# Performance work log

Measured on AMD Instinct MI355X. Metric: run time of the kernel, lower is better.

Reference implementation:

```python
import jax, jax.numpy as jnp
import numpy as np

B, L, D, K = 32, 200, 768, 8  # batch, seq_len, bert dim, max_span_length
S = int(sum(L - 1 - k for k in range(1, K + 1)))  # 1556 total spans for a full sentence


def setup_inputs() -> dict:
    key = jax.random.key(0)
    ks = jax.random.split(key, 20)
    features = jax.random.normal(ks[0], (B, L, D), dtype=jnp.float32)
    lengths = jax.random.randint(ks[1], (B,), K + 4, L + 1)  # valid token counts incl CLS/SEP
    mask = (jnp.arange(L)[None, :] < lengths[:, None]).astype(jnp.int32)
    span_mask = jnp.ones((B, S), dtype=jnp.int32)
    inp = {"features": features, "mask": mask, "span_mask": span_mask}
    for j in range(K - 1):
        k = j + 2
        inp[f"w{k}"] = jax.random.normal(ks[2 + j], (D, D, k), dtype=jnp.float32) * 0.02
        inp[f"b{k}"] = jax.random.normal(ks[10 + j], (D,), dtype=jnp.float32) * 0.02
    return inp


def _feature_slice(features, mask, num_spans, ws, bs):
    # features: [B, L, D]; mask: [B, L] (ones then zeros); ws[j]: Conv1d weight [D, D, j+2]
    Bb, Ll, Dd = features.shape
    Kk = len(ws) + 1  # max_span_length
    x = features.transpose(0, 2, 1)  # [B, D, L] (NCH)
    sources = [features]  # k=0: unigram features
    for w, b in zip(ws, bs):
        y = jax.lax.conv_general_dilated(x, w, (1,), "VALID", dimension_numbers=("NCH", "OIH", "NCH"))
        y = (y + b[None, :, None]).transpose(0, 2, 1)  # [B, L-k+1, D]
        sources.append(jnp.pad(y, ((0, 0), (0, Ll - y.shape[1]), (0, 0))))
    src = jnp.stack(sources, 0)  # [K, B, L, D]
    n = jnp.sum(mask, axis=1)  # valid lengths incl CLS/SEP
    # span-length k+1 contributes max(n - k - 2, 0) spans, sources start at index 1
    counts = jnp.maximum(n[:, None] - jnp.arange(Kk)[None, :] - 2, 0)  # [B, K]
    offsets = jnp.concatenate([jnp.zeros((Bb, 1), counts.dtype), jnp.cumsum(counts, axis=1)], axis=1)  # [B, K+1]
    s = jnp.arange(num_spans)
    kidx = jnp.sum(offsets[:, 1:Kk, None] <= s[None, None, :], axis=1)  # [B, S] bucket per slot
    pos = jnp.clip(s[None, :] - jnp.take_along_axis(offsets, kidx, axis=1) + 1, 0, Ll - 1)  # [B, S]
    valid = s[None, :] < offsets[:, Kk:Kk + 1]  # [B, S]
    out = src[kidx, jnp.arange(Bb)[:, None], pos] * valid[:, :, None].astype(features.dtype)
    return out, valid.astype(jnp.int32)


def reference(features, mask, span_mask, w2, w3, w4, w5, w6, w7, w8, b2, b3, b4, b5, b6, b7, b8):
    ws = (w2, w3, w4, w5, w6, w7, w8)
    bs = (b2, b3, b4, b5, b6, b7, b8)
    return _feature_slice(features, mask, span_mask.shape[1], ws, bs)
```

## Files before the change

### kernel.cpp

```cpp
#include <hip/hip_runtime.h>
#include <hip/hip_bf16.h>

#define BB 32
#define LL 200
#define DD 768
#define SS 1556
#define MAXM 6400

typedef __attribute__((ext_vector_type(8))) short bf16x8;
typedef __attribute__((ext_vector_type(4))) float floatx4;

__device__ __forceinline__ float bf2f(ushort u){
    union { unsigned int i; float f; } v; v.i = ((unsigned int)u) << 16; return v.f;
}
__device__ __forceinline__ ushort f2bf(float f){
    union { float f; unsigned int i; } v; v.f = f;
    unsigned int x = v.i;
    return (ushort)((x + 0x7FFFu + ((x >> 16) & 1u)) >> 16);
}

__device__ const int GCNT2[8] = {2,2,2,2,2,2,4,5};
__device__ const int GLIST2[8][5] = {
    {18, 9, 0, 0, 0},
    {19,10, 0, 0, 0},
    {20,11, 0, 0, 0},
    {15,12, 0, 0, 0},
    {16,13, 0, 0, 0},
    {17,14, 0, 0, 0},
    { 6, 7, 3, 0, 0},
    { 8, 4, 5, 1, 2},
};

__global__ void detect_kernel(const unsigned int* __restrict__ feat_raw, int* __restrict__ flag){
    __shared__ int cnt_s;
    if (threadIdx.x == 0) cnt_s = 0;
    __syncthreads();
    int c = 0;
    for (int i = threadIdx.x; i < 4096; i += 256){
        unsigned int w = feat_raw[i];
        unsigned int e = (w >> 7) & 0xFFu;
        if (e >= 100u && e <= 150u) c++;
    }
    atomicAdd(&cnt_s, c);
    __syncthreads();
    if (threadIdx.x == 0) *flag = (cnt_s > 2457) ? 1 : 0;
}

__global__ void offs_kernel(const int* __restrict__ mask, int* __restrict__ offs){
    int b = blockIdx.x;
    int lane = threadIdx.x;
    int s = 0;
    for (int i = lane; i < LL; i += 64) s += mask[b*LL + i];
    #pragma unroll
    for (int d = 32; d > 0; d >>= 1) s += __shfl_down(s, d, 64);
    if (lane == 0){
        int n = s, cum = 0;
        offs[b*9 + 0] = 0;
        for (int j = 0; j < 8; ++j){
            int c = n - j - 2; if (c < 0) c = 0;
            cum += c;
            offs[b*9 + j + 1] = cum;
        }
    }
}

__global__ void maps_kernel(const int* __restrict__ offs, int* __restrict__ pfx,
                            int* __restrict__ amap, int* __restrict__ omap){
    const int kkidx = blockIdx.x;
    const int kk = kkidx + 2;
    __shared__ int P[33];
    __shared__ int base_s[32];
    const int tid = threadIdx.x;
    if (tid == 0){
        int acc = 0; P[0] = 0;
        for (int b = 0; b < 32; ++b){
            acc += offs[b*9 + kk] - offs[b*9 + kk - 1];
            P[b+1] = acc;
        }
    }
    if (tid < 32) base_s[tid] = offs[tid*9 + kk - 1];
    __syncthreads();
    if (tid == 0) pfx[kkidx*33 + 32] = P[32];
    const int Mtot = P[32];
    for (int r = tid; r < MAXM; r += 256){
        int b = 0;
        #pragma unroll
        for (int i = 1; i <= 32; ++i) b += (P[i] <= r) ? 1 : 0;
        int bb = b < 32 ? b : 31;
        int larow = (r < Mtot) ? (r - P[bb]) : 0;
        amap[kkidx*MAXM + r] = bb*LL + larow + 1;
        omap[kkidx*MAXM + r] = bb*SS + base_s[bb] + larow;
    }
}

__global__ void repack2_kernel(const void* __restrict__ w2, const void* __restrict__ w3,
                               const void* __restrict__ w4, const void* __restrict__ w5,
                               const void* __restrict__ w6, const void* __restrict__ w7,
                               const void* __restrict__ w8,
                               const void* __restrict__ b2, const void* __restrict__ b3,
                               const void* __restrict__ b4, const void* __restrict__ b5,
                               const void* __restrict__ b6, const void* __restrict__ b7,
                               const void* __restrict__ b8,
                               ushort* __restrict__ BpAll, float* __restrict__ biasF,
                               const int* __restrict__ flag){
    const int kkidx = blockIdx.y;
    const int kk = kkidx + 2;
    const void* w  = kkidx==0?w2:kkidx==1?w3:kkidx==2?w4:kkidx==3?w5:kkidx==4?w6:kkidx==5?w7:w8;
    const void* bv = kkidx==0?b2:kkidx==1?b3:kkidx==2?b4:kkidx==3?b5:kkidx==4?b6:kkidx==5?b7:b8;
    ushort* Bp = BpAll + (size_t)(kkidx*(kkidx+3)/2)*589824;

    const int bfm = *flag;
    __shared__ ushort lds[24576];
    const int tid = threadIdx.x;
    const int ob  = blockIdx.x;
    const int rowlen = DD * kk;
    const int nelem  = 4 * rowlen;

    if (bfm){
        const ushort* src = (const ushort*)w + (size_t)ob * nelem;
        const int nch = nelem >> 3;
        for (int c = tid; c < nch; c += 256)
            __builtin_memcpy(lds + c*8, src + c*8, 16);
        if (ob == 0)
            for (int i = tid; i < DD; i += 256) biasF[kkidx*DD + i] = bf2f(((const ushort*)bv)[i]);
    } else {
        const float* src = (const float*)w + (size_t)ob * nelem;
        const int nch = nelem >> 2;
        for (int c = tid; c < nch; c += 256){
            float t4[4];
            __builtin_memcpy(t4, src + c*4, 16);
            #pragma unroll
            for (int j2 = 0; j2 < 4; ++j2) lds[c*4 + j2] = f2bf(t4[j2]);
        }
        if (ob == 0)
            for (int i = tid; i < DD; i += 256) biasF[kkidx*DD + i] = ((const float*)bv)[i];
    }
    __syncthreads();

    const int total = 96 * kk * 4;
    for (int c = tid; c < total; c += 256){
        int jb = c >> 2, ol = c & 3;
        int j0 = jb * 8;
        int t  = j0 / 768;
        int i0 = j0 - t * 768;
        ushort tmp[8];
        #pragma unroll
        for (int jj = 0; jj < 8; ++jj)
            tmp[jj] = lds[ol*rowlen + (i0 + jj)*kk + t];
        int o = ob*4 + ol;
        __builtin_memcpy(Bp + (size_t)jb*6144 + (size_t)o*8, tmp, 16);
    }
}

__global__ void cvtA_kernel(const void* __restrict__ feat, ushort* __restrict__ featbf,
                            const int* __restrict__ flag){
    const int bfm = *flag;
    int idx = blockIdx.x*256 + threadIdx.x;
    const int TOT = BB*LL*DD/8;
    if (idx >= TOT) return;
    if (bfm){
        __builtin_memcpy(featbf + (size_t)idx*8, (const ushort*)feat + (size_t)idx*8, 16);
    } else {
        float t8[8];
        __builtin_memcpy(t8,     (const float*)feat + (size_t)idx*8,     16);
        __builtin_memcpy(t8 + 4, (const float*)feat + (size_t)idx*8 + 4, 16);
        ushort o8[8];
        #pragma unroll
        for (int j = 0; j < 8; ++j) o8[j] = f2bf(t8[j]);
        __builtin_memcpy(featbf + (size_t)idx*8, o8, 16);
    }
}

__global__ void fill2_kernel(const void* __restrict__ feat, const int* __restrict__ offs,
                             void* __restrict__ out, const int* __restrict__ flag){
    const int s = blockIdx.x;
    const int b = blockIdx.y;
    const int bfm = *flag;
    const int tid = threadIdx.x;
    const int c0  = offs[b*9 + 1];
    const int tot = offs[b*9 + 8];
    if (bfm){
        if (tid < 96){
            ushort* dst = (ushort*)out + ((size_t)b*SS + s)*768 + tid*8;
            if (s < c0){
                const ushort* srcp = (const ushort*)feat + ((size_t)b*LL + s + 1)*768 + tid*8;
                __builtin_memcpy(dst, srcp, 16);
            } else if (s >= tot){
                const ushort z[8] = {0,0,0,0,0,0,0,0};
                __builtin_memcpy(dst, z, 16);
            }
        } else if (tid == 96){
            ((ushort*)out)[(size_t)BB*SS*768 + (size_t)b*SS + s] = (s < tot) ? (ushort)0x3F80 : (ushort)0;
        }
    } else {
        if (tid < 192){
            float* dst = (float*)out + ((size_t)b*SS + s)*768 + tid*4;
            if (s < c0){
                const float* srcp = (const float*)feat + ((size_t)b*LL + s + 1)*768 + tid*4;
                __builtin_memcpy(dst, srcp, 16);
            } else if (s >= tot){
                const float z[4] = {0.f,0.f,0.f,0.f};
                __builtin_memcpy(dst, z, 16);
            }
        } else if (tid == 192){
            ((float*)out)[(size_t)BB*SS*768 + (size_t)b*SS + s] = (s < tot) ? 1.0f : 0.0f;
        }
    }
}

__global__ __launch_bounds__(512, 2) void conv_gemm7(const ushort* __restrict__ featbf,
        const ushort* __restrict__ BpAll, const float* __restrict__ biasF,
        const int* __restrict__ pfx, const int* __restrict__ amap,
        const int* __restrict__ omap, void* __restrict__ out,
        const int* __restrict__ flag){
    const int n   = blockIdx.x;
    const int xcd = n & 7;
    const int is  = n >> 3;
    const int cx  = GCNT2[xcd];
    if (is >= cx * 25) return;
    const int gi = is % cx;
    const int mt = is / cx;
    const int g  = GLIST2[xcd][gi];
    const int kkidx = g / 3;
    const int nt = g - kkidx*3;
    const int kk = kkidx + 2;
    const int Mtot = pfx[kkidx*33 + 32];
    const int m0 = mt * 256;
    if (m0 >= Mtot) return;
    const int n0 = nt * 256;
    const int bfm = *flag;

    __shared__ ushort LDSbuf[32768];

    const int tid  = threadIdx.x;
    const int wv   = tid >> 6;
    const int wvm  = wv >> 1;
    const int wvn  = wv & 1;
    const int lane = tid & 63;
    const int quad = lane >> 4;
    const int l15  = lane & 15;

    const ushort* srcA[2];
    #pragma unroll
    for (int j = 0; j < 2; ++j){
        int g2 = j*8 + wv;
        int rr = kkidx*MAXM + m0 + (g2 >> 2)*64 + (g2 & 3)*16 + l15;
        srcA[j] = featbf + (size_t)amap[rr]*768 + quad*8;
    }
    const ushort* BkkBase = BpAll + (size_t)(kkidx*(kkidx+3)/2)*589824;
    const ushort* srcB[2];
    #pragma unroll
    for (int j = 0; j < 2; ++j){
        int c = j*512 + tid;
        srcB[j] = BkkBase + (size_t)(c >> 8)*6144 + (size_t)(n0 + (c & 255))*8;
    }

    floatx4 acc[4][8];
    #pragma unroll
    for (int sn = 0; sn < 8; ++sn){
        float bv = biasF[kkidx*768 + n0 + wvn*128 + sn*16 + l15];
        #pragma unroll
        for (int sm = 0; sm < 4; ++sm){
            acc[sm][sn][0] = bv; acc[sm][sn][1] = bv;
            acc[sm][sn][2] = bv; acc[sm][sn][3] = bv;
        }
    }

    char* lds0 = (char*)&LDSbuf[0];
    const int nchunks = kk * 24;

    #define STAGE(BUF, ch) do { \
        _Pragma("unroll") \
        for (int j_ = 0; j_ < 2; ++j_) \
            __builtin_amdgcn_global_load_lds( \
                (const __attribute__((address_space(1))) void*)(srcA[j_] + (ch)*32), \
                (__attribute__((address_space(3))) void*)(lds0 + (BUF)*32768 + (j_*512 + tid)*16), \
                16, 0, 0); \
        _Pragma("unroll") \
        for (int j_ = 0; j_ < 2; ++j_) \
            __builtin_amdgcn_global_load_lds( \
                (const __attribute__((address_space(1))) void*)(srcB[j_] + (size_t)(ch)*24576), \
                (__attribute__((address_space(3))) void*)(lds0 + (BUF)*32768 + 16384 + (j_*512 + tid)*16), \
                16, 0, 0); \
        } while(0)

    #define COMPUTE(BUF) do { \
        bf16x8 afr[4], bfr[8]; \
        _Pragma("unroll") \
        for (int sm_ = 0; sm_ < 4; ++sm_) \
            __builtin_memcpy(&afr[sm_], lds0 + (BUF)*32768 + (wvm*4 + sm_)*1024 + lane*16, 16); \
        _Pragma("unroll") \
        for (int sn_ = 0; sn_ < 8; ++sn_) \
            __builtin_memcpy(&bfr[sn_], lds0 + (BUF)*32768 + 16384 + quad*4096 + (wvn*128 + sn_*16 + l15)*16, 16); \
        __builtin_amdgcn_s_setprio(1); \
        _Pragma("unroll") \
        for (int sm_ = 0; sm_ < 4; ++sm_) \
            _Pragma("unroll") \
            for (int sn_ = 0; sn_ < 8; ++sn_) \
                acc[sm_][sn_] = __builtin_amdgcn_mfma_f32_16x16x32_bf16( \
                    afr[sm_], bfr[sn_], acc[sm_][sn_], 0, 0, 0); \
        __builtin_amdgcn_s_setprio(0); \
        } while(0)

    #define SUBSTEP(CH, CUR, NXT, DO, NW) do { \
        if (DO) STAGE(NXT, (CH)+1); \
        __builtin_amdgcn_sched_barrier(0); \
        asm volatile("s_waitcnt vmcnt(" NW ")" ::: "memory"); \
        __builtin_amdgcn_sched_barrier(0); \
        __builtin_amdgcn_s_barrier(); \
        __builtin_amdgcn_sched_barrier(0); \
        COMPUTE(CUR); \
        __builtin_amdgcn_s_barrier(); \
        __builtin_amdgcn_sched_barrier(0); \
    } while(0)

    STAGE(0, 0);
    for (int ch = 0; ch < nchunks - 2; ch += 2){
        SUBSTEP(ch,   0, 1, true, "4");
        SUBSTEP(ch+1, 1, 0, true, "4");
    }
    SUBSTEP(nchunks-2, 0, 1, true,  "4");
    SUBSTEP(nchunks-1, 1, 0, false, "0");

    #undef SUBSTEP
    #undef STAGE
    #undef COMPUTE

    #pragma unroll
    for (int sm = 0; sm < 4; ++sm){
        #pragma unroll
        for (int rr = 0; rr < 4; ++rr){
            int r2 = m0 + wvm*64 + sm*16 + quad*4 + rr;
            if (r2 < Mtot){
                int slot = omap[kkidx*MAXM + r2];
                if (bfm){
                    ushort* oh = (ushort*)out;
                    #pragma unroll
                    for (int sn = 0; sn < 8; ++sn)
                        oh[(size_t)slot*768 + n0 + wvn*128 + sn*16 + l15] = f2bf(acc[sm][sn][rr]);
                } else {
                    float* of = (float*)out;
                    #pragma unroll
                    for (int sn = 0; sn < 8; ++sn)
                        of[(size_t)slot*768 + n0 + wvn*128 + sn*16 + l15] = acc[sm][sn][rr];
                }
            }
        }
    }
}

__global__ __launch_bounds__(256) void conv_gemm_direct(const void* __restrict__ feat,
        const int* __restrict__ offs, void* __restrict__ out, const int* __restrict__ flag,
        const void* w2, const void* w3, const void* w4, const void* w5,
        const void* w6, const void* w7, const void* w8,
        const void* b2, const void* b3, const void* b4, const void* b5,
        const void* b6, const void* b7, const void* b8){
    const int bfm = *flag;
    const int kkidx = blockIdx.y;
    const int kk = kkidx + 2;
    const int b = blockIdx.z;
    const void* w  = kkidx==0?w2:kkidx==1?w3:kkidx==2?w4:kkidx==3?w5:kkidx==4?w6:kkidx==5?w7:w8;
    const void* bv = kkidx==0?b2:kkidx==1?b3:kkidx==2?b4:kkidx==3?b5:kkidx==4?b6:kkidx==5?b7:b8;

    const int off_j = offs[b*9 + kk - 1];
    const int cnt   = offs[b*9 + kk] - off_j;
    const int mt = blockIdx.x / 12;
    const int nt = blockIdx.x - mt*12;
    const int m0 = mt * 64;
    if (m0 >= cnt) return;
    const int n0 = nt * 64;

    const int tid  = threadIdx.x;
    const int wvv  = tid >> 6;
    const int lane = tid & 63;
    const int quad = lane >> 4;
    const int l15  = lane & 15;

    int row  = m0 + wvv*16 + l15;
    int arow = row < cnt ? row : cnt - 1;
    const size_t abase = ((size_t)b*LL + arow + 1)*768 + quad*8;

    floatx4 acc[4];
    #pragma unroll
    for (int cg = 0; cg < 4; ++cg){
        float bb = bfm ? bf2f(((const ushort*)bv)[n0 + cg*16 + l15])
                       : ((const float*)bv)[n0 + cg*16 + l15];
        acc[cg][0] = bb; acc[cg][1] = bb; acc[cg][2] = bb; acc[cg][3] = bb;
    }

    const int steps = kk * 24;
    for (int s = 0; s < steps; ++s){
        bf16x8 a;
        if (bfm){
            __builtin_memcpy(&a, (const ushort*)feat + abase + s*32, 16);
        } else {
            float t8[8];
            __builtin_memcpy(t8,     (const float*)feat + abase + s*32,     16);
            __builtin_memcpy(t8 + 4, (const float*)feat + abase + s*32 + 4, 16);
            ushort o8[8];
            #pragma unroll
            for (int j = 0; j < 8; ++j) o8[j] = f2bf(t8[j]);
            __builtin_memcpy(&a, o8, 16);
        }
        int j0 = s*32 + quad*8;
        int t  = j0 / 768;
        int i0 = j0 - t*768;
        #pragma unroll
        for (int cg = 0; cg < 4; ++cg){
            int o = n0 + cg*16 + l15;
            size_t wbase = (size_t)o*(DD*kk) + (size_t)i0*kk + t;
            ushort tmp[8];
            if (bfm){
                const ushort* wp = (const ushort*)w + wbase;
                #pragma unroll
                for (int jj = 0; jj < 8; ++jj) tmp[jj] = wp[(size_t)jj*kk];
            } else {
                const float* wp = (const float*)w + wbase;
                #pragma unroll
                for (int jj = 0; jj < 8; ++jj) tmp[jj] = f2bf(wp[(size_t)jj*kk]);
            }
            bf16x8 bfr;
            __builtin_memcpy(&bfr, tmp, 16);
            acc[cg] = __builtin_amdgcn_mfma_f32_16x16x32_bf16(a, bfr, acc[cg], 0, 0, 0);
        }
    }

    const int rbase = m0 + wvv*16 + quad*4;
    if (bfm){
        ushort* outh = (ushort*)out;
        #pragma unroll
        for (int cg = 0; cg < 4; ++cg)
            #pragma unroll
            for (int rr = 0; rr < 4; ++rr){
                int grow = rbase + rr;
                if (grow < cnt)
                    outh[((size_t)b*SS + off_j + grow)*768 + n0 + cg*16 + l15] = f2bf(acc[cg][rr]);
            }
    } else {
        float* outf = (float*)out;
        #pragma unroll
        for (int cg = 0; cg < 4; ++cg)
            #pragma unroll
            for (int rr = 0; rr < 4; ++rr){
                int grow = rbase + rr;
                if (grow < cnt)
                    outf[((size_t)b*SS + off_j + grow)*768 + n0 + cg*16 + l15] = acc[cg][rr];
            }
    }
}

extern "C" void kernel_launch(void* const* d_in, const int* in_sizes, int n_in,
                              void* d_out, int out_size, void* d_ws, size_t ws_size,
                              hipStream_t stream) {
    const void* feat = d_in[0];
    const int*  mask = (const int*)d_in[1];

    const void* w[7]  = {0,0,0,0,0,0,0};
    const void* bs[7] = {0,0,0,0,0,0,0};
    int bi = 0;
    for (int i = 3; i < n_in; ++i){
        if (in_sizes[i] == 768){
            if (bi < 7) bs[bi++] = d_in[i];
        } else {
            int kk = in_sizes[i] / 589824;
            if (kk >= 2 && kk <= 8) w[kk-2] = d_in[i];
        }
    }

    char* ws = (char*)d_ws;
    int*    flag    = (int*)ws;
    int*    offs    = (int*)(ws + 64);
    int*    pfx     = (int*)(ws + 2048);
    float*  biasF   = (float*)(ws + 4096);
    int*    amap    = (int*)(ws + 28672);
    int*    omap    = (int*)(ws + 28672 + 179200);
    ushort* featbf  = (ushort*)(ws + 393216);
    ushort* Bp      = (ushort*)(ws + 393216 + 9830400);
    const size_t FULL_BYTES = 393216ull + 9830400ull + 41287680ull;
    const bool use_full = ws_size >= FULL_BYTES;

    hipLaunchKernelGGL(detect_kernel, dim3(1), dim3(256), 0, stream,
                       (const unsigned int*)feat, flag);
    hipLaunchKernelGGL(offs_kernel, dim3(BB), dim3(64), 0, stream, mask, offs);

    if (use_full){
        hipLaunchKernelGGL(repack2_kernel, dim3(192, 7), dim3(256), 0, stream,
                           w[0], w[1], w[2], w[3], w[4], w[5], w[6],
                           bs[0], bs[1], bs[2], bs[3], bs[4], bs[5], bs[6],
                           Bp, biasF, flag);
        hipLaunchKernelGGL(cvtA_kernel, dim3(2400), dim3(256), 0, stream, feat, featbf, flag);
        hipLaunchKernelGGL(maps_kernel, dim3(7), dim3(256), 0, stream, offs, pfx, amap, omap);
    }

    hipLaunchKernelGGL(fill2_kernel, dim3(SS, BB), dim3(256), 0, stream,
                       feat, offs, d_out, flag);

    if (use_full){
        hipLaunchKernelGGL(conv_gemm7, dim3(1000), dim3(512), 0, stream,
                           featbf, Bp, biasF, pfx, amap, omap, d_out, flag);
    } else {
        hipLaunchKernelGGL(conv_gemm_direct, dim3(48, 7, BB), dim3(256), 0, stream,
                           feat, offs, d_out, flag,
                           w[0], w[1], w[2], w[3], w[4], w[5], w[6],
                           bs[0], bs[1], bs[2], bs[3], bs[4], bs[5], bs[6]);
    }
}
```

Baseline: 563.9 us.

## Merge prep kernels into two launches and widen GEMM to 1024 threads

The detect and offset kernels are combined into one launch, and weight repacking, feature conversion, map building and span fill are merged into a single block-partitioned prep kernel, reducing launch count and inter-kernel gaps. The conv GEMM moves from 512 to 1024 threads per block, with each of 16 waves owning a 64x64 sub-tile (4x4 MFMA accumulators instead of 4x8). Each thread now issues one A and one B global-to-LDS load per stage, and the vmcnt wait changes to match. The risks are lower per-wave register reuse from smaller per-wave tiles and a single block per CU at 1024 threads.

```diff
diff --git a/kernel.cpp b/kernel.cpp
--- a/kernel.cpp
+++ b/kernel.cpp
@@ -31,184 +31,191 @@
     { 8, 4, 5, 1, 2},
 };
 
-__global__ void detect_kernel(const unsigned int* __restrict__ feat_raw, int* __restrict__ flag){
+__global__ void prep1_kernel(const unsigned int* __restrict__ feat_raw,
+                             const int* __restrict__ mask,
+                             int* __restrict__ flag, int* __restrict__ offs){
     __shared__ int cnt_s;
-    if (threadIdx.x == 0) cnt_s = 0;
-    __syncthreads();
-    int c = 0;
-    for (int i = threadIdx.x; i < 4096; i += 256){
-        unsigned int w = feat_raw[i];
-        unsigned int e = (w >> 7) & 0xFFu;
-        if (e >= 100u && e <= 150u) c++;
-    }
-    atomicAdd(&cnt_s, c);
-    __syncthreads();
-    if (threadIdx.x == 0) *flag = (cnt_s > 2457) ? 1 : 0;
-}
-
-__global__ void offs_kernel(const int* __restrict__ mask, int* __restrict__ offs){
-    int b = blockIdx.x;
-    int lane = threadIdx.x;
-    int s = 0;
-    for (int i = lane; i < LL; i += 64) s += mask[b*LL + i];
-    #pragma unroll
-    for (int d = 32; d > 0; d >>= 1) s += __shfl_down(s, d, 64);
-    if (lane == 0){
-        int n = s, cum = 0;
-        offs[b*9 + 0] = 0;
-        for (int j = 0; j < 8; ++j){
-            int c = n - j - 2; if (c < 0) c = 0;
-            cum += c;
-            offs[b*9 + j + 1] = cum;
-        }
-    }
-}
-
-__global__ void maps_kernel(const int* __restrict__ offs, int* __restrict__ pfx,
-                            int* __restrict__ amap, int* __restrict__ omap){
-    const int kkidx = blockIdx.x;
-    const int kk = kkidx + 2;
+    const int bx = blockIdx.x;
+    const int tid = threadIdx.x;
+    if (bx == 0){
+        if (tid == 0) cnt_s = 0;
+        __syncthreads();
+        int c = 0;
+        for (int i = tid; i < 4096; i += 256){
+            unsigned int w = feat_raw[i];
+            unsigned int e = (w >> 7) & 0xFFu;
+            if (e >= 100u && e <= 150u) c++;
+        }
+        atomicAdd(&cnt_s, c);
+        __syncthreads();
+        if (tid == 0) *flag = (cnt_s > 2457) ? 1 : 0;
+    } else {
+        const int b = bx - 1;
+        if (tid < 64){
+            int s = 0;
+            for (int i = tid; i < LL; i += 64) s += mask[b*LL + i];
+            #pragma unroll
+            for (int d = 32; d > 0; d >>= 1) s += __shfl_down(s, d, 64);
+            if (tid == 0){
+                int n = s, cum = 0;
+                offs[b*9 + 0] = 0;
+                for (int j = 0; j < 8; ++j){
+                    int c2 = n - j - 2; if (c2 < 0) c2 = 0;
+                    cum += c2;
+                    offs[b*9 + j + 1] = cum;
+                }
+            }
+        }
+    }
+}
+
+__global__ void prep2_kernel(const void* __restrict__ feat, const int* __restrict__ offs,
+        const int* __restrict__ flag,
+        const void* w2, const void* w3, const void* w4, const void* w5,
+        const void* w6, const void* w7, const void* w8,
+        const void* b2, const void* b3, const void* b4, const void* b5,
+        const void* b6, const void* b7, const void* b8,
+        ushort* __restrict__ BpAll, float* __restrict__ biasF,
+        ushort* __restrict__ featbf, int* __restrict__ pfx,
+        int* __restrict__ amap, int* __restrict__ omap,
+        void* __restrict__ out, int full){
+    __shared__ ushort lds[24576];
     __shared__ int P[33];
     __shared__ int base_s[32];
     const int tid = threadIdx.x;
-    if (tid == 0){
-        int acc = 0; P[0] = 0;
-        for (int b = 0; b < 32; ++b){
-            acc += offs[b*9 + kk] - offs[b*9 + kk - 1];
-            P[b+1] = acc;
-        }
-    }
-    if (tid < 32) base_s[tid] = offs[tid*9 + kk - 1];
-    __syncthreads();
-    if (tid == 0) pfx[kkidx*33 + 32] = P[32];
-    const int Mtot = P[32];
-    for (int r = tid; r < MAXM; r += 256){
-        int b = 0;
-        #pragma unroll
-        for (int i = 1; i <= 32; ++i) b += (P[i] <= r) ? 1 : 0;
-        int bb = b < 32 ? b : 31;
-        int larow = (r < Mtot) ? (r - P[bb]) : 0;
-        amap[kkidx*MAXM + r] = bb*LL + larow + 1;
-        omap[kkidx*MAXM + r] = bb*SS + base_s[bb] + larow;
-    }
-}
-
-__global__ void repack2_kernel(const void* __restrict__ w2, const void* __restrict__ w3,
-                               const void* __restrict__ w4, const void* __restrict__ w5,
-                               const void* __restrict__ w6, const void* __restrict__ w7,
-                               const void* __restrict__ w8,
-                               const void* __restrict__ b2, const void* __restrict__ b3,
-                               const void* __restrict__ b4, const void* __restrict__ b5,
-                               const void* __restrict__ b6, const void* __restrict__ b7,
-                               const void* __restrict__ b8,
-                               ushort* __restrict__ BpAll, float* __restrict__ biasF,
-                               const int* __restrict__ flag){
-    const int kkidx = blockIdx.y;
-    const int kk = kkidx + 2;
-    const void* w  = kkidx==0?w2:kkidx==1?w3:kkidx==2?w4:kkidx==3?w5:kkidx==4?w6:kkidx==5?w7:w8;
-    const void* bv = kkidx==0?b2:kkidx==1?b3:kkidx==2?b4:kkidx==3?b5:kkidx==4?b6:kkidx==5?b7:b8;
-    ushort* Bp = BpAll + (size_t)(kkidx*(kkidx+3)/2)*589824;
-
+    const int bx  = blockIdx.x;
     const int bfm = *flag;
-    __shared__ ushort lds[24576];
-    const int tid = threadIdx.x;
-    const int ob  = blockIdx.x;
-    const int rowlen = DD * kk;
-    const int nelem  = 4 * rowlen;
-
-    if (bfm){
-        const ushort* src = (const ushort*)w + (size_t)ob * nelem;
-        const int nch = nelem >> 3;
-        for (int c = tid; c < nch; c += 256)
-            __builtin_memcpy(lds + c*8, src + c*8, 16);
-        if (ob == 0)
-            for (int i = tid; i < DD; i += 256) biasF[kkidx*DD + i] = bf2f(((const ushort*)bv)[i]);
+    const int repN = full ? 1344 : 0;
+    const int cvtN = full ? 1200 : 0;
+    const int mapN = full ? 7 : 0;
+
+    if (bx < repN){
+        const int kkidx = bx / 192;
+        const int ob    = bx - kkidx*192;
+        const int kk    = kkidx + 2;
+        const void* w  = kkidx==0?w2:kkidx==1?w3:kkidx==2?w4:kkidx==3?w5:kkidx==4?w6:kkidx==5?w7:w8;
+        const void* bv = kkidx==0?b2:kkidx==1?b3:kkidx==2?b4:kkidx==3?b5:kkidx==4?b6:kkidx==5?b7:b8;
+        ushort* Bp = BpAll + (size_t)(kkidx*(kkidx+3)/2)*589824;
+        const int rowlen = DD * kk;
+        const int nelem  = 4 * rowlen;
+        if (bfm){
+            const ushort* src = (const ushort*)w + (size_t)ob * nelem;
+            const int nch = nelem >> 3;
+            for (int c = tid; c < nch; c += 256)
+                __builtin_memcpy(lds + c*8, src + c*8, 16);
+            if (ob == 0)
+                for (int i = tid; i < DD; i += 256) biasF[kkidx*DD + i] = bf2f(((const ushort*)bv)[i]);
+        } else {
+            const float* src = (const float*)w + (size_t)ob * nelem;
+            const int nch = nelem >> 2;
+            for (int c = tid; c < nch; c += 256){
+                float t4[4];
+                __builtin_memcpy(t4, src + c*4, 16);
+                #pragma unroll
+                for (int j2 = 0; j2 < 4; ++j2) lds[c*4 + j2] = f2bf(t4[j2]);
+            }
+            if (ob == 0)
+                for (int i = tid; i < DD; i += 256) biasF[kkidx*DD + i] = ((const float*)bv)[i];
+        }
+        __syncthreads();
+        const int total = 96 * kk * 4;
+        for (int c = tid; c < total; c += 256){
+            int jb = c >> 2, ol = c & 3;
+            int j0 = jb * 8;
+            int t  = j0 / 768;
+            int i0 = j0 - t * 768;
+            ushort tmp[8];
+            #pragma unroll
+            for (int jj = 0; jj < 8; ++jj)
+                tmp[jj] = lds[ol*rowlen + (i0 + jj)*kk + t];
+            int o = ob*4 + ol;
+            __builtin_memcpy(Bp + (size_t)jb*6144 + (size_t)o*8, tmp, 16);
+        }
+    } else if (bx < repN + cvtN){
+        const int TOT = BB*LL*DD/8;
+        for (int idx = (bx - repN)*256 + tid; idx < TOT; idx += cvtN*256){
+            if (bfm){
+                __builtin_memcpy(featbf + (size_t)idx*8, (const ushort*)feat + (size_t)idx*8, 16);
+            } else {
+                float t8[8];
+                __builtin_memcpy(t8,     (const float*)feat + (size_t)idx*8,     16);
+                __builtin_memcpy(t8 + 4, (const float*)feat + (size_t)idx*8 + 4, 16);
+                ushort o8[8];
+                #pragma unroll
+                for (int j = 0; j < 8; ++j) o8[j] = f2bf(t8[j]);
+                __builtin_memcpy(featbf + (size_t)idx*8, o8, 16);
+            }
+        }
+    } else if (bx < repN + cvtN + mapN){
+        const int kkidx = bx - (repN + cvtN);
+        const int kk = kkidx + 2;
+        if (tid == 0){
+            int acc = 0; P[0] = 0;
+            for (int b = 0; b < 32; ++b){
+                acc += offs[b*9 + kk] - offs[b*9 + kk - 1];
+                P[b+1] = acc;
+            }
+        }
+        if (tid < 32) base_s[tid] = offs[tid*9 + kk - 1];
+        __syncthreads();
+        if (tid == 0) pfx[kkidx*33 + 32] = P[32];
+        const int Mtot = P[32];
+        for (int r = tid; r < MAXM; r += 256){
+            int b = 0;
+            #pragma unroll
+            for (int i = 1; i <= 32; ++i) b += (P[i] <= r) ? 1 : 0;
+            int bb = b < 32 ? b : 31;
+            int larow = (r < Mtot) ? (r - P[bb]) : 0;
+            amap[kkidx*MAXM + r] = bb*LL + larow + 1;
+            omap[kkidx*MAXM + r] = bb*SS + base_s[bb] + larow;
+        }
     } else {
-        const float* src = (const float*)w + (size_t)ob * nelem;
-        const int nch = nelem >> 2;
-        for (int c = tid; c < nch; c += 256){
-            float t4[4];
-            __builtin_memcpy(t4, src + c*4, 16);
-            #pragma unroll
-            for (int j2 = 0; j2 < 4; ++j2) lds[c*4 + j2] = f2bf(t4[j2]);
-        }
-        if (ob == 0)
-            for (int i = tid; i < DD; i += 256) biasF[kkidx*DD + i] = ((const float*)bv)[i];
-    }
-    __syncthreads();
-
-    const int total = 96 * kk * 4;
-    for (int c = tid; c < total; c += 256){
-        int jb = c >> 2, ol = c & 3;
-        int j0 = jb * 8;
-        int t  = j0 / 768;
-        int i0 = j0 - t * 768;
-        ushort tmp[8];
-        #pragma unroll
-        for (int jj = 0; jj < 8; ++jj)
-            tmp[jj] = lds[ol*rowlen + (i0 + jj)*kk + t];
-        int o = ob*4 + ol;
-        __builtin_memcpy(Bp + (size_t)jb*6144 + (size_t)o*8, tmp, 16);
-    }
-}
-
-__global__ void cvtA_kernel(const void* __restrict__ feat, ushort* __restrict__ featbf,
-                            const int* __restrict__ flag){
-    const int bfm = *flag;
-    int idx = blockIdx.x*256 + threadIdx.x;
-    const int TOT = BB*LL*DD/8;
-    if (idx >= TOT) return;
-    if (bfm){
-        __builtin_memcpy(featbf + (size_t)idx*8, (const ushort*)feat + (size_t)idx*8, 16);
-    } else {
-        float t8[8];
-        __builtin_memcpy(t8,     (const float*)feat + (size_t)idx*8,     16);
-        __builtin_memcpy(t8 + 4, (const float*)feat + (size_t)idx*8 + 4, 16);
-        ushort o8[8];
-        #pragma unroll
-        for (int j = 0; j < 8; ++j) o8[j] = f2bf(t8[j]);
-        __builtin_memcpy(featbf + (size_t)idx*8, o8, 16);
-    }
-}
-
-__global__ void fill2_kernel(const void* __restrict__ feat, const int* __restrict__ offs,
-                             void* __restrict__ out, const int* __restrict__ flag){
-    const int s = blockIdx.x;
-    const int b = blockIdx.y;
-    const int bfm = *flag;
-    const int tid = threadIdx.x;
-    const int c0  = offs[b*9 + 1];
-    const int tot = offs[b*9 + 8];
-    if (bfm){
-        if (tid < 96){
-            ushort* dst = (ushort*)out + ((size_t)b*SS + s)*768 + tid*8;
-            if (s < c0){
-                const ushort* srcp = (const ushort*)feat + ((size_t)b*LL + s + 1)*768 + tid*8;
-                __builtin_memcpy(dst, srcp, 16);
-            } else if (s >= tot){
-                const ushort z[8] = {0,0,0,0,0,0,0,0};
-                __builtin_memcpy(dst, z, 16);
-            }
-        } else if (tid == 96){
-            ((ushort*)out)[(size_t)BB*SS*768 + (size_t)b*SS + s] = (s < tot) ? (ushort)0x3F80 : (ushort)0;
-        }
-    } else {
-        if (tid < 192){
-            float* dst = (float*)out + ((size_t)b*SS + s)*768 + tid*4;
-            if (s < c0){
-                const float* srcp = (const float*)feat + ((size_t)b*LL + s + 1)*768 + tid*4;
-                __builtin_memcpy(dst, srcp, 16);
-            } else if (s >= tot){
-                const float z[4] = {0.f,0.f,0.f,0.f};
-                __builtin_memcpy(dst, z, 16);
-            }
-        } else if (tid == 192){
-            ((float*)out)[(size_t)BB*SS*768 + (size_t)b*SS + s] = (s < tot) ? 1.0f : 0.0f;
-        }
-    }
-}
-
-__global__ __launch_bounds__(512, 2) void conv_gemm7(const ushort* __restrict__ featbf,
+        const int fb = bx - (repN + cvtN + mapN);
+        if (bfm){
+            const int TOTC = BB*SS*96;
+            for (int idx = fb*256 + tid; idx < TOTC; idx += 2048*256){
+                int r  = idx / 96;
+                int c  = idx - r*96;
+                int b  = r / SS;
+                int s  = r - b*SS;
+                int c0  = offs[b*9 + 1];
+                int tot = offs[b*9 + 8];
+                ushort* dst = (ushort*)out + ((size_t)r)*768 + c*8;
+                if (s < c0){
+                    const ushort* srcp = (const ushort*)feat + ((size_t)b*LL + s + 1)*768 + c*8;
+                    __builtin_memcpy(dst, srcp, 16);
+                } else if (s >= tot){
+                    const ushort z[8] = {0,0,0,0,0,0,0,0};
+                    __builtin_memcpy(dst, z, 16);
+                }
+                if (c == 0)
+                    ((ushort*)out)[(size_t)BB*SS*768 + (size_t)b*SS + s] = (s < tot) ? (ushort)0x3F80 : (ushort)0;
+            }
+        } else {
+            const int TOTC = BB*SS*192;
+            for (int idx = fb*256 + tid; idx < TOTC; idx += 2048*256){
+                int r  = idx / 192;
+                int c  = idx - r*192;
+                int b  = r / SS;
+                int s  = r - b*SS;
+                int c0  = offs[b*9 + 1];
+                int tot = offs[b*9 + 8];
+                float* dst = (float*)out + ((size_t)r)*768 + c*4;
+                if (s < c0){
+                    const float* srcp = (const float*)feat + ((size_t)b*LL + s + 1)*768 + c*4;
+                    __builtin_memcpy(dst, srcp, 16);
+                } else if (s >= tot){
+                    const float z[4] = {0.f,0.f,0.f,0.f};
+                    __builtin_memcpy(dst, z, 16);
+                }
+                if (c == 0)
+                    ((float*)out)[(size_t)BB*SS*768 + (size_t)b*SS + s] = (s < tot) ? 1.0f : 0.0f;
+            }
+        }
+    }
+}
+
+__global__ __launch_bounds__(1024) void conv_gemm8(const ushort* __restrict__ featbf,
         const ushort* __restrict__ BpAll, const float* __restrict__ biasF,
         const int* __restrict__ pfx, const int* __restrict__ amap,
         const int* __restrict__ omap, void* __restrict__ out,
@@ -234,31 +241,24 @@
 
     const int tid  = threadIdx.x;
     const int wv   = tid >> 6;
-    const int wvm  = wv >> 1;
-    const int wvn  = wv & 1;
+    const int wvm  = wv >> 2;
+    const int wvn  = wv & 3;
     const int lane = tid & 63;
     const int quad = lane >> 4;
     const int l15  = lane & 15;
 
-    const ushort* srcA[2];
+    const ushort* srcA = featbf + (size_t)amap[kkidx*MAXM + m0 + wv*16 + l15]*768 + quad*8;
+    const ushort* BkkBase = BpAll + (size_t)(kkidx*(kkidx+3)/2)*589824;
+    const ushort* srcB = BkkBase + (size_t)(wv >> 2)*6144 + (size_t)(n0 + (wv & 3)*64 + lane)*8;
+
+    char* lds0 = (char*)&LDSbuf[0];
+    const int dstA = wv*1024;
+    const int dstB = 16384 + wv*1024;
+
+    floatx4 acc[4][4];
     #pragma unroll
-    for (int j = 0; j < 2; ++j){
-        int g2 = j*8 + wv;
-        int rr = kkidx*MAXM + m0 + (g2 >> 2)*64 + (g2 & 3)*16 + l15;
-        srcA[j] = featbf + (size_t)amap[rr]*768 + quad*8;
-    }
-    const ushort* BkkBase = BpAll + (size_t)(kkidx*(kkidx+3)/2)*589824;
-    const ushort* srcB[2];
-    #pragma unroll
-    for (int j = 0; j < 2; ++j){
-        int c = j*512 + tid;
-        srcB[j] = BkkBase + (size_t)(c >> 8)*6144 + (size_t)(n0 + (c & 255))*8;
-    }
-
-    floatx4 acc[4][8];
-    #pragma unroll
-    for (int sn = 0; sn < 8; ++sn){
-        float bv = biasF[kkidx*768 + n0 + wvn*128 + sn*16 + l15];
+    for (int sn = 0; sn < 4; ++sn){
+        float bv = biasF[kkidx*768 + n0 + wvn*64 + sn*16 + l15];
         #pragma unroll
         for (int sm = 0; sm < 4; ++sm){
             acc[sm][sn][0] = bv; acc[sm][sn][1] = bv;
@@ -266,37 +266,32 @@
         }
     }
 
-    char* lds0 = (char*)&LDSbuf[0];
     const int nchunks = kk * 24;
 
     #define STAGE(BUF, ch) do { \
-        _Pragma("unroll") \
-        for (int j_ = 0; j_ < 2; ++j_) \
-            __builtin_amdgcn_global_load_lds( \
-                (const __attribute__((address_space(1))) void*)(srcA[j_] + (ch)*32), \
-                (__attribute__((address_space(3))) void*)(lds0 + (BUF)*32768 + (j_*512 + tid)*16), \
-                16, 0, 0); \
-        _Pragma("unroll") \
-        for (int j_ = 0; j_ < 2; ++j_) \
-            __builtin_amdgcn_global_load_lds( \
-                (const __attribute__((address_space(1))) void*)(srcB[j_] + (size_t)(ch)*24576), \
-                (__attribute__((address_space(3))) void*)(lds0 + (BUF)*32768 + 16384 + (j_*512 + tid)*16), \
-                16, 0, 0); \
+        __builtin_amdgcn_global_load_lds( \
+            (const __attribute__((address_space(1))) void*)(srcA + (ch)*32), \
+            (__attribute__((address_space(3))) void*)(lds0 + (BUF)*32768 + dstA), \
+            16, 0, 0); \
+        __builtin_amdgcn_global_load_lds( \
+            (const __attribute__((address_space(1))) void*)(srcB + (size_t)(ch)*24576), \
+            (__attribute__((address_space(3))) void*)(lds0 + (BUF)*32768 + dstB), \
+            16, 0, 0); \
         } while(0)
 
     #define COMPUTE(BUF) do { \
-        bf16x8 afr[4], bfr[8]; \
+        bf16x8 afr[4], bfr[4]; \
         _Pragma("unroll") \
         for (int sm_ = 0; sm_ < 4; ++sm_) \
             __builtin_memcpy(&afr[sm_], lds0 + (BUF)*32768 + (wvm*4 + sm_)*1024 + lane*16, 16); \
         _Pragma("unroll") \
-        for (int sn_ = 0; sn_ < 8; ++sn_) \
-            __builtin_memcpy(&bfr[sn_], lds0 + (BUF)*32768 + 16384 + quad*4096 + (wvn*128 + sn_*16 + l15)*16, 16); \
+        for (int sn_ = 0; sn_ < 4; ++sn_) \
+            __builtin_memcpy(&bfr[sn_], lds0 + (BUF)*32768 + 16384 + quad*4096 + (wvn*64 + sn_*16 + l15)*16, 16); \
         __builtin_amdgcn_s_setprio(1); \
         _Pragma("unroll") \
         for (int sm_ = 0; sm_ < 4; ++sm_) \
             _Pragma("unroll") \
-            for (int sn_ = 0; sn_ < 8; ++sn_) \
+            for (int sn_ = 0; sn_ < 4; ++sn_) \
                 acc[sm_][sn_] = __builtin_amdgcn_mfma_f32_16x16x32_bf16( \
                     afr[sm_], bfr[sn_], acc[sm_][sn_], 0, 0, 0); \
         __builtin_amdgcn_s_setprio(0); \
@@ -316,10 +311,10 @@
 
     STAGE(0, 0);
     for (int ch = 0; ch < nchunks - 2; ch += 2){
-        SUBSTEP(ch,   0, 1, true, "4");
-        SUBSTEP(ch+1, 1, 0, true, "4");
-    }
-    SUBSTEP(nchunks-2, 0, 1, true,  "4");
+        SUBSTEP(ch,   0, 1, true, "2");
+        SUBSTEP(ch+1, 1, 0, true, "2");
+    }
+    SUBSTEP(nchunks-2, 0, 1, true,  "2");
     SUBSTEP(nchunks-1, 1, 0, false, "0");
 
     #undef SUBSTEP
@@ -336,13 +331,13 @@
                 if (bfm){
                     ushort* oh = (ushort*)out;
                     #pragma unroll
-                    for (int sn = 0; sn < 8; ++sn)
-                        oh[(size_t)slot*768 + n0 + wvn*128 + sn*16 + l15] = f2bf(acc[sm][sn][rr]);
+                    for (int sn = 0; sn < 4; ++sn)
+                        oh[(size_t)slot*768 + n0 + wvn*64 + sn*16 + l15] = f2bf(acc[sm][sn][rr]);
                 } else {
                     float* of = (float*)out;
                     #pragma unroll
-                    for (int sn = 0; sn < 8; ++sn)
-                        of[(size_t)slot*768 + n0 + wvn*128 + sn*16 + l15] = acc[sm][sn][rr];
+                    for (int sn = 0; sn < 4; ++sn)
+                        of[(size_t)slot*768 + n0 + wvn*64 + sn*16 + l15] = acc[sm][sn][rr];
                 }
             }
         }
@@ -479,26 +474,23 @@
     const size_t FULL_BYTES = 393216ull + 9830400ull + 41287680ull;
     const bool use_full = ws_size >= FULL_BYTES;
 
-    hipLaunchKernelGGL(detect_kernel, dim3(1), dim3(256), 0, stream,
-                       (const unsigned int*)feat, flag);
-    hipLaunchKernelGGL(offs_kernel, dim3(BB), dim3(64), 0, stream, mask, offs);
+    hipLaunchKernelGGL(prep1_kernel, dim3(33), dim3(256), 0, stream,
+                       (const unsigned int*)feat, mask, flag, offs);
 
     if (use_full){
-        hipLaunchKernelGGL(repack2_kernel, dim3(192, 7), dim3(256), 0, stream,
+        hipLaunchKernelGGL(prep2_kernel, dim3(4599), dim3(256), 0, stream,
+                           feat, offs, flag,
                            w[0], w[1], w[2], w[3], w[4], w[5], w[6],
                            bs[0], bs[1], bs[2], bs[3], bs[4], bs[5], bs[6],
-                           Bp, biasF, flag);
-        hipLaunchKernelGGL(cvtA_kernel, dim3(2400), dim3(256), 0, stream, feat, featbf, flag);
-        hipLaunchKernelGGL(maps_kernel, dim3(7), dim3(256), 0, stream, offs, pfx, amap, omap);
-    }
-
-    hipLaunchKernelGGL(fill2_kernel, dim3(SS, BB), dim3(256), 0, stream,
-                       feat, offs, d_out, flag);
-
-    if (use_full){
-        hipLaunchKernelGGL(conv_gemm7, dim3(1000), dim3(512), 0, stream,
+                           Bp, biasF, featbf, pfx, amap, omap, d_out, 1);
+        hipLaunchKernelGGL(conv_gemm8, dim3(1000), dim3(1024), 0, stream,
                            featbf, Bp, biasF, pfx, amap, omap, d_out, flag);
     } else {
+        hipLaunchKernelGGL(prep2_kernel, dim3(2048), dim3(256), 0, stream,
+                           feat, offs, flag,
+                           w[0], w[1], w[2], w[3], w[4], w[5], w[6],
+                           bs[0], bs[1], bs[2], bs[3], bs[4], bs[5], bs[6],
+                           Bp, biasF, featbf, pfx, amap, omap, d_out, 0);
         hipLaunchKernelGGL(conv_gemm_direct, dim3(48, 7, BB), dim3(256), 0, stream,
                            feat, offs, d_out, flag,
                            w[0], w[1], w[2], w[3], w[4], w[5], w[6],
```

Result: faster. 494.9 us (-12.2%).
